# Kernel tuning notes

Hardware: AMD Instinct MI355X
Metric: run time of the kernel (lower is better)

## Reference

```python
import jax, jax.numpy as jnp
import numpy as np

B, C, H, W = 64, 512, 7, 7        # x4: dim_b=512, layer4 spatial 7x7
HY, WY = 28, 28                   # y (x1): layer1 56x56 -> cov1 stride2 -> 28x28
NUM_HEADS = 8
HEAD_DIM = C // NUM_HEADS
SCALE = HEAD_DIM ** -0.5
K1, K2 = 2, 3
LN_EPS = 1e-5


def _avgpool_same(y, k, p):
    # torch nn.AvgPool2d(kernel=k, stride=1, padding=p), count_include_pad=True
    s = jax.lax.reduce_window(y, 0.0, jax.lax.add, (1, 1, k, k), (1, 1, 1, 1),
                              [(0, 0), (0, 0), (p, p), (p, p)])
    return s / float(k * k)


def setup_inputs() -> dict:
    key = jax.random.key(0)
    ks = jax.random.split(key, 8)
    x = jax.random.normal(ks[0], (B, C, H, W), dtype=jnp.float32)
    y = jax.random.normal(ks[1], (B, C, HY, WY), dtype=jnp.float32)
    # Linear weights stored as [in, out] (apply via x @ W)
    Wq = jax.random.normal(ks[2], (C, C), dtype=jnp.float32) * 0.02
    Wkv = jax.random.normal(ks[3], (C, 2 * C), dtype=jnp.float32) * 0.02
    Wproj = jax.random.normal(ks[4], (C, C), dtype=jnp.float32) * 0.02
    bproj = jnp.zeros((C,), dtype=jnp.float32)
    gamma = jnp.ones((C,), dtype=jnp.float32)
    beta = jnp.zeros((C,), dtype=jnp.float32)
    attn_w1 = jnp.full((1,), 0.5, dtype=jnp.float32)
    attn_w2 = jnp.full((1,), 0.5, dtype=jnp.float32)
    return dict(x=x, y=y, Wq=Wq, Wkv=Wkv, Wproj=Wproj, bproj=bproj,
                gamma=gamma, beta=beta, attn_w1=attn_w1, attn_w2=attn_w2)


def _topk_masked_softmax(attn, kc):
    # torch: scatter top-kc indices into a 0/1 mask, then where(mask>0, attn, -inf).
    # Equivalent (tie-free, as with continuous random logits): keep entries >= kth value.
    thr = jax.lax.top_k(attn, kc)[0][..., -1:]
    masked = jnp.where(attn >= jax.lax.stop_gradient(thr), attn, -jnp.inf)
    return jax.nn.softmax(masked, axis=-1)


def reference(x, y, Wq, Wkv, Wproj, bproj, gamma, beta, attn_w1, attn_w2):
    # Multi-scale pooling on y (all stride 1, 'same' spatial size)
    y = _avgpool_same(y, 3, 1) + _avgpool_same(y, 5, 2) + _avgpool_same(y, 7, 3)
    N1 = HY * WY
    y = y.reshape(B, C, N1).transpose(0, 2, 1)          # [B, N1, C]
    # LayerNorm over C
    mu = jnp.mean(y, axis=-1, keepdims=True)
    var = jnp.var(y, axis=-1, keepdims=True)
    y = (y - mu) / jnp.sqrt(var + LN_EPS) * gamma + beta

    N = H * W
    xs = x.reshape(B, C, N).transpose(0, 2, 1)          # [B, N, C]

    kv = (y @ Wkv).reshape(B, N1, 2, NUM_HEADS, HEAD_DIM)
    kv = kv.transpose(2, 0, 3, 1, 4)                    # [2, B, h, N1, d]
    k, v = kv[0], kv[1]
    q = (xs @ Wq).reshape(B, N, NUM_HEADS, HEAD_DIM).transpose(0, 2, 1, 3)  # [B,h,N,d]

    attn = jnp.einsum('bhnd,bhmd->bhnm', q, k) * SCALE  # [B, h, N, N1]

    attn1 = _topk_masked_softmax(attn, N1 // K1)
    attn2 = _topk_masked_softmax(attn, N1 // K2)
    out1 = jnp.einsum('bhnm,bhmd->bhnd', attn1, v)
    out2 = jnp.einsum('bhnm,bhmd->bhnd', attn2, v)
    out = out1 * attn_w1 + out2 * attn_w2               # [B, h, N, d]

    out = out.transpose(0, 2, 1, 3).reshape(B, N, C)    # [B, N, C]
    out = out @ Wproj + bproj
    return out.transpose(0, 2, 1).reshape(B, C, H, W)
```

## Files before the change

### kernel.cpp

```cpp
#include <hip/hip_runtime.h>
#include <hip/hip_bf16.h>


typedef __hip_bfloat16 bf16;
using bf16x8 = __attribute__((ext_vector_type(8))) short;
using f32x4 = __attribute__((ext_vector_type(4))) float;

#define DI __device__ __forceinline__

DI unsigned short b2u(float f) {
  bf16 h = __float2bfloat16(f);
  return *reinterpret_cast<unsigned short*>(&h);
}
DI float u2f(short s) { return __uint_as_float(((unsigned int)(unsigned short)s) << 16); }

DI float unkey(unsigned int k) {
  unsigned int u = (k & 0x80000000u) ? (k & 0x7FFFFFFFu) : ~k;
  return __uint_as_float(u);
}

__global__ __launch_bounds__(256) void pool2t_kernel(const float* __restrict__ y,
                                                     bf16* __restrict__ pooledT) {
  const int b = blockIdx.x >> 6, cg = blockIdx.x & 63;
  const float* src = y + ((size_t)b * 512 + cg * 8) * 784;
  bf16* drow = pooledT + ((size_t)b * 784) * 512 + cg * 8;
  __shared__ float I[8][870];
  const int tid = threadIdx.x;
  for (int i = tid; i < 6272; i += 256) {
    int p = i / 784, j = i - p * 784;
    int r = j / 28, c = j - r * 28;
    I[p][(r + 1) * 30 + c + 1] = src[p * 784 + j];
  }
  for (int i = tid; i < 8 * 58; i += 256) {
    int p = i / 58, e = i - p * 58;
    if (e < 30) I[p][e] = 0.f;
    else I[p][(e - 29) * 30] = 0.f;
  }
  __syncthreads();
  if (tid < 224) {
    int p = tid / 28, r = tid - (tid / 28) * 28;
    float run = 0.f;
    float* row = &I[p][(r + 1) * 30 + 1];
#pragma unroll
    for (int c = 0; c < 28; ++c) { run += row[c]; row[c] = run; }
  }
  __syncthreads();
  if (tid < 224) {
    int p = tid / 28, c = tid - (tid / 28) * 28;
    float run = 0.f;
    float* col = &I[p][30 + c + 1];
#pragma unroll
    for (int r = 0; r < 28; ++r) { run += col[r * 30]; col[r * 30] = run; }
  }
  __syncthreads();
  for (int j = tid; j < 784; j += 256) {
    int r = j / 28, c = j - (j / 28) * 28;
    int r0[3], r1[3], c0[3], c1[3];
#pragma unroll
    for (int pk = 1; pk <= 3; ++pk) {
      r0[pk - 1] = max(r - pk, 0) * 30;
      r1[pk - 1] = (min(r + pk, 27) + 1) * 30;
      c0[pk - 1] = max(c - pk, 0);
      c1[pk - 1] = min(c + pk, 27) + 1;
    }
    unsigned int u[4];
#pragma unroll
    for (int q = 0; q < 4; ++q) {
      float vv[2];
#pragma unroll
      for (int t = 0; t < 2; ++t) {
        const float* Ip = I[q * 2 + t];
        float acc = 0.f;
#pragma unroll
        for (int k = 0; k < 3; ++k) {
          float s = Ip[r1[k] + c1[k]] - Ip[r0[k] + c1[k]] - Ip[r1[k] + c0[k]] + Ip[r0[k] + c0[k]];
          acc += s * ((k == 0) ? (1.f / 9.f) : (k == 1) ? (1.f / 25.f) : (1.f / 49.f));
        }
        vv[t] = acc;
      }
      u[q] = (unsigned int)b2u(vv[0]) | ((unsigned int)b2u(vv[1]) << 16);
    }
    *reinterpret_cast<uint4*>(drow + (size_t)j * 512) = make_uint4(u[0], u[1], u[2], u[3]);
  }
}

__global__ __launch_bounds__(256) void lnrow_kernel(const bf16* __restrict__ pooledT,
                                                    const float* __restrict__ gamma,
                                                    const float* __restrict__ beta,
                                                    bf16* __restrict__ yln) {
  const int row = blockIdx.x * 4 + (threadIdx.x >> 6);
  const int lane = threadIdx.x & 63;
  bf16x8 raw = *reinterpret_cast<const bf16x8*>(pooledT + (size_t)row * 512 + lane * 8);
  float v[8];
  float s = 0.f, s2 = 0.f;
#pragma unroll
  for (int j = 0; j < 8; ++j) {
    v[j] = u2f(raw[j]);
    s += v[j];
    s2 += v[j] * v[j];
  }
#pragma unroll
  for (int off = 32; off; off >>= 1) {
    s += __shfl_xor(s, off, 64);
    s2 += __shfl_xor(s2, off, 64);
  }
  float mu = s * (1.f / 512.f);
  float rs = rsqrtf(s2 * (1.f / 512.f) - mu * mu + 1e-5f);
  float4 g0 = *reinterpret_cast<const float4*>(gamma + lane * 8);
  float4 g1 = *reinterpret_cast<const float4*>(gamma + lane * 8 + 4);
  float4 e0 = *reinterpret_cast<const float4*>(beta + lane * 8);
  float4 e1 = *reinterpret_cast<const float4*>(beta + lane * 8 + 4);
  float gg[8] = {g0.x, g0.y, g0.z, g0.w, g1.x, g1.y, g1.z, g1.w};
  float bb[8] = {e0.x, e0.y, e0.z, e0.w, e1.x, e1.y, e1.z, e1.w};
  unsigned int u[4];
#pragma unroll
  for (int q = 0; q < 4; ++q) {
    float o0 = (v[2 * q] - mu) * rs * gg[2 * q] + bb[2 * q];
    float o1 = (v[2 * q + 1] - mu) * rs * gg[2 * q + 1] + bb[2 * q + 1];
    u[q] = (unsigned int)b2u(o0) | ((unsigned int)b2u(o1) << 16);
  }
  *reinterpret_cast<uint4*>(yln + (size_t)row * 512 + lane * 8) = make_uint4(u[0], u[1], u[2], u[3]);
}

__global__ __launch_bounds__(256) void prep_kernel(const float* __restrict__ Wkv,
                                                   const float* __restrict__ Wq,
                                                   const float* __restrict__ Wproj,
                                                   const float* __restrict__ x,
                                                   bf16* __restrict__ wkvT, bf16* __restrict__ wqT,
                                                   bf16* __restrict__ wpT, bf16* __restrict__ xsTb,
                                                   bf16* __restrict__ Vt) {
  __shared__ float t[32][33];
  const int blk = blockIdx.x;
  const int tid = threadIdx.x;
  if (blk < 1024) {
    const float* W;
    bf16* WT;
    int N, bx, by;
    if (blk < 512) { W = Wkv; WT = wkvT; N = 1024; bx = blk & 31; by = blk >> 5; }
    else if (blk < 768) { W = Wq; WT = wqT; N = 512; bx = (blk - 512) & 15; by = (blk - 512) >> 4; }
    else { W = Wproj; WT = wpT; N = 512; bx = (blk - 768) & 15; by = (blk - 768) >> 4; }
    const int n0 = bx * 32, k0 = by * 32;
    for (int i = tid; i < 1024; i += 256) {
      int kr = i >> 5, nc = i & 31;
      t[kr][nc] = W[(size_t)(k0 + kr) * N + n0 + nc];
    }
    __syncthreads();
    for (int i = tid; i < 1024; i += 256) {
      int nr = i >> 5, kc = i & 31;
      WT[(size_t)(n0 + nr) * 512 + k0 + kc] = __float2bfloat16(t[kc][nr]);
    }
  } else if (blk < 7296) {
    int idx = (blk - 1024) * 256 + tid;
    int c = idx & 511;
    int rem = idx >> 9;
    int r = rem % 49, b = rem / 49;
    xsTb[idx] = __float2bfloat16(x[((size_t)b * 512 + c) * 49 + r]);
  } else {
    int idx = (blk - 7296) * 256 + tid;
    int row = idx >> 4, c = idx & 15;
    Vt[(size_t)row * 800 + 784 + c] = __float2bfloat16(0.f);
  }
}

#define GLD_LDS16(g, l)                                                              \
  __builtin_amdgcn_global_load_lds((const __attribute__((address_space(1))) unsigned int*)(g), \
                                   (__attribute__((address_space(3))) unsigned int*)(l), 16, 0, 0)

__global__ __launch_bounds__(256) void kv_mfma(const bf16* __restrict__ A,
                                               const bf16* __restrict__ Bt,
                                               bf16* __restrict__ Kb, bf16* __restrict__ Vt) {
  extern __shared__ __align__(16) bf16 smem[];
  bf16* As = smem;
  bf16* Bs = smem + 128 * 32;
  const int tid = threadIdx.x;
  const int lane = tid & 63;
  const int w = tid >> 6, wr = w >> 1, wc = w & 1;

  const int lin = blockIdx.y * 8 + blockIdx.x;
  const int c8 = lin & 7, j = lin >> 3;
  const int ex = j & 7, ey = c8 * 49 + (j >> 3);
  const int m0 = ey * 128, n0 = ex * 128;

  f32x4 acc[4][4];
#pragma unroll
  for (int m = 0; m < 4; ++m)
#pragma unroll
    for (int n = 0; n < 4; ++n) acc[m][n] = f32x4{0.f, 0.f, 0.f, 0.f};

  const int s0 = tid, s1 = tid + 256;
  const bf16* Ag0 = A + (size_t)(m0 + (s0 >> 2)) * 512 + (s0 & 3) * 8;
  const bf16* Ag1 = A + (size_t)(m0 + (s1 >> 2)) * 512 + (s1 & 3) * 8;
  const bf16* Bg0 = Bt + (size_t)(n0 + (s0 >> 2)) * 512 + (s0 & 3) * 8;
  const bf16* Bg1 = Bt + (size_t)(n0 + (s1 >> 2)) * 512 + (s1 & 3) * 8;
  bf16* Al0 = As + s0 * 8;
  bf16* Al1 = As + s1 * 8;
  bf16* Bl0 = Bs + s0 * 8;
  bf16* Bl1 = Bs + s1 * 8;

  const int fr = lane & 15;
  const int ko = (lane >> 4) * 8;
  const int rh = lane >> 4;

  for (int k0 = 0; k0 < 512; k0 += 32) {
    GLD_LDS16(Ag0 + k0, Al0);
    GLD_LDS16(Ag1 + k0, Al1);
    GLD_LDS16(Bg0 + k0, Bl0);
    GLD_LDS16(Bg1 + k0, Bl1);
    __syncthreads();
    bf16x8 af[4], bfr[4];
#pragma unroll
    for (int m = 0; m < 4; ++m)
      af[m] = *reinterpret_cast<const bf16x8*>(As + (wr * 64 + m * 16 + fr) * 32 + ko);
#pragma unroll
    for (int n = 0; n < 4; ++n)
      bfr[n] = *reinterpret_cast<const bf16x8*>(Bs + (wc * 64 + n * 16 + fr) * 32 + ko);
#pragma unroll
    for (int m = 0; m < 4; ++m)
#pragma unroll
      for (int n = 0; n < 4; ++n)
        acc[m][n] = __builtin_amdgcn_mfma_f32_16x16x32_bf16(af[m], bfr[n], acc[m][n], 0, 0, 0);
    __syncthreads();
  }

  if (n0 < 512) {
#pragma unroll
    for (int m = 0; m < 4; ++m) {
#pragma unroll
      for (int n = 0; n < 4; ++n) {
        int col = n0 + wc * 64 + n * 16 + fr;
        const size_t cbase = ((size_t)(col >> 6)) * (784 * 64) + (col & 63);
#pragma unroll
        for (int r = 0; r < 4; ++r) {
          int row = m0 + wr * 64 + m * 16 + rh * 4 + r;
          int b = row / 784, n1 = row - (row / 784) * 784;
          Kb[((size_t)b * 8) * (784 * 64) + cbase + (size_t)n1 * 64] = __float2bfloat16(acc[m][n][r]);
        }
      }
    }
  } else {
    bf16* stage = smem;
#pragma unroll
    for (int p = 0; p < 2; ++p) {
      __syncthreads();
      if (wr == p) {
#pragma unroll
        for (int m = 0; m < 4; ++m) {
#pragma unroll
          for (int n = 0; n < 4; ++n) {
            int coll = wc * 64 + n * 16 + fr;
            int rowl = m * 16 + rh * 4;
            unsigned int u0 = (unsigned int)b2u(acc[m][n][0]) | ((unsigned int)b2u(acc[m][n][1]) << 16);
            unsigned int u1 = (unsigned int)b2u(acc[m][n][2]) | ((unsigned int)b2u(acc[m][n][3]) << 16);
            *reinterpret_cast<uint2*>(stage + coll * 72 + rowl) = make_uint2(u0, u1);
          }
        }
      }
      __syncthreads();
      const int rbase = m0 + p * 64;
      for (int i = tid; i < 1024; i += 256) {
        int cc = i >> 3, tc = i & 7;
        int colg = n0 + cc;
        int h = (colg >> 6) & 7, d = colg & 63;
        int rs = rbase + tc * 8;
        int b = rs / 784, n1 = rs - b * 784;
        bf16x8 val = *reinterpret_cast<const bf16x8*>(stage + cc * 72 + tc * 8);
        bf16* dst = Vt + (((size_t)b * 8 + h) * 64 + d) * 800 + n1;
        if (n1 <= 776) {
          *reinterpret_cast<bf16x8*>(dst) = val;
        } else {
#pragma unroll
          for (int jj = 0; jj < 8; ++jj) {
            int rr = rs + jj;
            int bb2 = rr / 784, nn1 = rr - bb2 * 784;
            bf16 hv;
            *reinterpret_cast<short*>(&hv) = val[jj];
            Vt[(((size_t)bb2 * 8 + h) * 64 + d) * 800 + nn1] = hv;
          }
        }
      }
    }
  }
}

__global__ __launch_bounds__(256) void q_mfma(const bf16* __restrict__ A,
                                              const bf16* __restrict__ Bt,
                                              bf16* __restrict__ Qb) {
  __shared__ __align__(16) bf16 As[128 * 32];
  __shared__ __align__(16) bf16 Bs[128 * 32];
  const int tid = threadIdx.x;
  const int lane = tid & 63;
  const int w = tid >> 6, wr = w >> 1, wc = w & 1;
  const int m0 = blockIdx.y * 128, n0 = blockIdx.x * 128;

  f32x4 acc[4][4];
#pragma unroll
  for (int m = 0; m < 4; ++m)
#pragma unroll
    for (int n = 0; n < 4; ++n) acc[m][n] = f32x4{0.f, 0.f, 0.f, 0.f};

  const int s0 = tid, s1 = tid + 256;
  const bf16* Ag0 = A + (size_t)(m0 + (s0 >> 2)) * 512 + (s0 & 3) * 8;
  const bf16* Ag1 = A + (size_t)(m0 + (s1 >> 2)) * 512 + (s1 & 3) * 8;
  const bf16* Bg0 = Bt + (size_t)(n0 + (s0 >> 2)) * 512 + (s0 & 3) * 8;
  const bf16* Bg1 = Bt + (size_t)(n0 + (s1 >> 2)) * 512 + (s1 & 3) * 8;
  bf16* Al0 = As + s0 * 8;
  bf16* Al1 = As + s1 * 8;
  bf16* Bl0 = Bs + s0 * 8;
  bf16* Bl1 = Bs + s1 * 8;

  const int fr = lane & 15;
  const int ko = (lane >> 4) * 8;
  const int rh = lane >> 4;

  for (int k0 = 0; k0 < 512; k0 += 32) {
    GLD_LDS16(Ag0 + k0, Al0);
    GLD_LDS16(Ag1 + k0, Al1);
    GLD_LDS16(Bg0 + k0, Bl0);
    GLD_LDS16(Bg1 + k0, Bl1);
    __syncthreads();
    bf16x8 af[4], bfr[4];
#pragma unroll
    for (int m = 0; m < 4; ++m)
      af[m] = *reinterpret_cast<const bf16x8*>(As + (wr * 64 + m * 16 + fr) * 32 + ko);
#pragma unroll
    for (int n = 0; n < 4; ++n)
      bfr[n] = *reinterpret_cast<const bf16x8*>(Bs + (wc * 64 + n * 16 + fr) * 32 + ko);
#pragma unroll
    for (int m = 0; m < 4; ++m)
#pragma unroll
      for (int n = 0; n < 4; ++n)
        acc[m][n] = __builtin_amdgcn_mfma_f32_16x16x32_bf16(af[m], bfr[n], acc[m][n], 0, 0, 0);
    __syncthreads();
  }

#pragma unroll
  for (int m = 0; m < 4; ++m) {
#pragma unroll
    for (int n = 0; n < 4; ++n) {
      int col = n0 + wc * 64 + n * 16 + fr;
      const size_t cbase = ((size_t)(col >> 6)) * (49 * 64) + (col & 63);
#pragma unroll
      for (int r = 0; r < 4; ++r) {
        int row = m0 + wr * 64 + m * 16 + rh * 4 + r;
        if (row < 3136) {
          int b = row / 49, rr = row - (row / 49) * 49;
          Qb[((size_t)b * 8) * (49 * 64) + cbase + (size_t)rr * 64] = __float2bfloat16(acc[m][n][r]);
        }
      }
    }
  }
}

__global__ __launch_bounds__(256) void proj_mfma(const bf16* __restrict__ A,
                                                 const bf16* __restrict__ Bt,
                                                 const float* __restrict__ bias,
                                                 float* __restrict__ out) {
  __shared__ __align__(16) bf16 As[128 * 32];
  __shared__ __align__(16) bf16 Bs[128 * 32];
  const int tid = threadIdx.x;
  const int lane = tid & 63;
  const int w = tid >> 6, wr = w >> 1, wc = w & 1;
  const int m0 = blockIdx.y * 128, n0 = blockIdx.x * 128;

  f32x4 acc[4][4];
#pragma unroll
  for (int m = 0; m < 4; ++m)
#pragma unroll
    for (int n = 0; n < 4; ++n) acc[m][n] = f32x4{0.f, 0.f, 0.f, 0.f};

  const int s0 = tid, s1 = tid + 256;
  const bf16* Ag0 = A + (size_t)(m0 + (s0 >> 2)) * 1024 + (s0 & 3) * 8;
  const bf16* Ag1 = A + (size_t)(m0 + (s1 >> 2)) * 1024 + (s1 & 3) * 8;
  const bf16* Bg0 = Bt + (size_t)(n0 + (s0 >> 2)) * 512 + (s0 & 3) * 8;
  const bf16* Bg1 = Bt + (size_t)(n0 + (s1 >> 2)) * 512 + (s1 & 3) * 8;
  bf16* Al0 = As + s0 * 8;
  bf16* Al1 = As + s1 * 8;
  bf16* Bl0 = Bs + s0 * 8;
  bf16* Bl1 = Bs + s1 * 8;

  const int fr = lane & 15;
  const int ko = (lane >> 4) * 8;
  const int rh = lane >> 4;

  for (int k0 = 0; k0 < 1024; k0 += 32) {
    GLD_LDS16(Ag0 + k0, Al0);
    GLD_LDS16(Ag1 + k0, Al1);
    GLD_LDS16(Bg0 + (k0 & 511), Bl0);
    GLD_LDS16(Bg1 + (k0 & 511), Bl1);
    __syncthreads();
    bf16x8 af[4], bfr[4];
#pragma unroll
    for (int m = 0; m < 4; ++m)
      af[m] = *reinterpret_cast<const bf16x8*>(As + (wr * 64 + m * 16 + fr) * 32 + ko);
#pragma unroll
    for (int n = 0; n < 4; ++n)
      bfr[n] = *reinterpret_cast<const bf16x8*>(Bs + (wc * 64 + n * 16 + fr) * 32 + ko);
#pragma unroll
    for (int m = 0; m < 4; ++m)
#pragma unroll
      for (int n = 0; n < 4; ++n)
        acc[m][n] = __builtin_amdgcn_mfma_f32_16x16x32_bf16(af[m], bfr[n], acc[m][n], 0, 0, 0);
    __syncthreads();
  }

#pragma unroll
  for (int m = 0; m < 4; ++m) {
#pragma unroll
    for (int n = 0; n < 4; ++n) {
      int col = n0 + wc * 64 + n * 16 + fr;
      float bv = bias[col];
#pragma unroll
      for (int r = 0; r < 4; ++r) {
        int row = m0 + wr * 64 + m * 16 + rh * 4 + r;
        if (row < 3136) {
          int b = row / 49, rr = row - (row / 49) * 49;
          out[((size_t)b * 512 + col) * 49 + rr] = acc[m][n][r] + bv;
        }
      }
    }
  }
}

__global__ __launch_bounds__(256, 7) void attn_kernel(const bf16* __restrict__ Qb,
                                                      const bf16* __restrict__ K,
                                                      const bf16* __restrict__ Vt,
                                                      const float* __restrict__ aw1p,
                                                      const float* __restrict__ aw2p,
                                                      bf16* __restrict__ aoutHL) {
  const int lin = blockIdx.x;
  const int wk = (lin & 7) * 448 + (lin >> 3);
  const int bh = wk / 7;
  const int chunk = wk - bh * 7;
  const int b = bh >> 3, h = bh & 7;
  const int r0 = chunk * 7;
  const int tid = threadIdx.x;
  const int lane = tid & 63, w = tid >> 6;
  __shared__ __align__(16) unsigned char sMem[21952];
  float* sLog = reinterpret_cast<float*>(sMem);
  bf16* sW = reinterpret_cast<bf16*>(sMem);

  const int fr = lane & 15, ko = (lane >> 4) * 8, rh = lane >> 4;

  const bf16* Qp = Qb + ((size_t)bh * 49 + r0) * 64;
  const int qrow = (fr < 7) ? fr : 6;
  const bf16x8 aq0 = *reinterpret_cast<const bf16x8*>(Qp + qrow * 64 + ko);
  const bf16x8 aq1 = *reinterpret_cast<const bf16x8*>(Qp + qrow * 64 + 32 + ko);

  const bf16* Kp = K + (size_t)bh * (784 * 64);
  {
    const int rbase = rh * 4;
    const bf16* kbase = Kp + (size_t)fr * 64 + ko;
    bf16x8 kq0[4], kq1[4];
#pragma unroll
    for (int s = 0; s < 4; ++s) {
      int nt = w + s * 4;
      int ntc = nt < 49 ? nt : 48;
      const bf16* kr = kbase + (size_t)ntc * 1024;
      kq0[s] = *reinterpret_cast<const bf16x8*>(kr);
      kq1[s] = *reinterpret_cast<const bf16x8*>(kr + 32);
    }
#pragma unroll
    for (int i = 0; i < 13; ++i) {
      const int s = i & 3;
      const int nt = w + i * 4;
      if (nt < 49) {
        f32x4 acc = {0.f, 0.f, 0.f, 0.f};
        acc = __builtin_amdgcn_mfma_f32_16x16x32_bf16(aq0, kq0[s], acc, 0, 0, 0);
        acc = __builtin_amdgcn_mfma_f32_16x16x32_bf16(aq1, kq1[s], acc, 0, 0, 0);
#pragma unroll
        for (int r = 0; r < 4; ++r) {
          int row = rbase + r;
          if (row < 7) sLog[row * 784 + nt * 16 + fr] = acc[r] * 0.125f;
        }
      }
      const int ntn = w + (i + 4) * 4;
      if (ntn < 49) {
        const bf16* kr = kbase + (size_t)ntn * 1024;
        kq0[s] = *reinterpret_cast<const bf16x8*>(kr);
        kq1[s] = *reinterpret_cast<const bf16x8*>(kr + 32);
      }
    }
  }
  __syncthreads();

  const int ra = w;
  const int rb = (w + 4 < 7) ? (w + 4) : w;
  float va[13], vb[13];
#pragma unroll
  for (int i = 0; i < 13; ++i) {
    int m = lane + i * 64;
    va[i] = (m < 784) ? sLog[ra * 784 + m] : -INFINITY;
    vb[i] = (m < 784) ? sLog[rb * 784 + m] : -INFINITY;
  }
  __syncthreads();

  float mxa = va[0], mxb = vb[0];
#pragma unroll
  for (int i = 1; i < 13; ++i) {
    mxa = fmaxf(mxa, va[i]);
    mxb = fmaxf(mxb, vb[i]);
  }
#pragma unroll
  for (int off = 32; off; off >>= 1) {
    mxa = fmaxf(mxa, __shfl_xor(mxa, off, 64));
    mxb = fmaxf(mxb, __shfl_xor(mxb, off, 64));
  }

  unsigned int t1a = 0u, t2a = 0u, t1b = 0u, t2b = 0u;
  bool d1a = false, d2a = false, d1b = false, d2b = false;
  for (int bit = 31; bit >= 0; --bit) {
    const unsigned int mb = 1u << bit;
    if (!d1a) {
      float cf = unkey(t1a | mb);
      int n = 0;
#pragma unroll
      for (int i = 0; i < 13; ++i) n += __popcll(__ballot(va[i] >= cf));
      if (n >= 392) { t1a |= mb; d1a = (n == 392); }
    }
    if (!d2a) {
      float cf = unkey(t2a | mb);
      int n = 0;
#pragma unroll
      for (int i = 0; i < 13; ++i) n += __popcll(__ballot(va[i] >= cf));
      if (n >= 261) { t2a |= mb; d2a = (n == 261); }
    }
    if (!d1b) {
      float cf = unkey(t1b | mb);
      int n = 0;
#pragma unroll
      for (int i = 0; i < 13; ++i) n += __popcll(__ballot(vb[i] >= cf));
      if (n >= 392) { t1b |= mb; d1b = (n == 392); }
    }
    if (!d2b) {
      float cf = unkey(t2b | mb);
      int n = 0;
#pragma unroll
      for (int i = 0; i < 13; ++i) n += __popcll(__ballot(vb[i] >= cf));
      if (n >= 261) { t2b |= mb; d2b = (n == 261); }
    }
    if (d1a & d2a & d1b & d2b) break;
  }
  const float T1a = unkey(t1a), T2a = unkey(t2a);
  const float T1b = unkey(t1b), T2b = unkey(t2b);

  const float aw1 = aw1p[0], aw2 = aw2p[0];
  float ea[13], eb[13];
  float z1a = 0.f, z2a = 0.f, z1b = 0.f, z2b = 0.f;
#pragma unroll
  for (int i = 0; i < 13; ++i) {
    ea[i] = __expf(va[i] - mxa);
    eb[i] = __expf(vb[i] - mxb);
    if (va[i] >= T1a) z1a += ea[i];
    if (va[i] >= T2a) z2a += ea[i];
    if (vb[i] >= T1b) z1b += eb[i];
    if (vb[i] >= T2b) z2b += eb[i];
  }
#pragma unroll
  for (int off = 32; off; off >>= 1) {
    z1a += __shfl_xor(z1a, off, 64);
    z2a += __shfl_xor(z2a, off, 64);
    z1b += __shfl_xor(z1b, off, 64);
    z2b += __shfl_xor(z2b, off, 64);
  }
  const float a1a = aw1 / z1a, a2a = aw2 / z2a;
  const float a1b = aw1 / z1b, a2b = aw2 / z2b;
#pragma unroll
  for (int i = 0; i < 13; ++i) {
    int m = lane + i * 64;
    if (m < 784) {
      float wa = ea[i] * (((va[i] >= T1a) ? a1a : 0.f) + ((va[i] >= T2a) ? a2a : 0.f));
      sW[ra * 808 + m] = __float2bfloat16(wa);
      float wb = eb[i] * (((vb[i] >= T1b) ? a1b : 0.f) + ((vb[i] >= T2b) ? a2b : 0.f));
      sW[rb * 808 + m] = __float2bfloat16(wb);
    }
  }
  if (lane < 16) {
    sW[ra * 808 + 784 + lane] = __float2bfloat16(0.f);
    sW[rb * 808 + 784 + lane] = __float2bfloat16(0.f);
  }

  const bf16* vbase = Vt + ((size_t)bh * 64 + w * 16 + fr) * 800;
  bf16x8 vq[4];
#pragma unroll
  for (int s = 0; s < 4; ++s)
    vq[s] = *reinterpret_cast<const bf16x8*>(vbase + s * 32 + ko);
  __syncthreads();

  const bf16* wrow = sW + ((fr < 7) ? fr : 7) * 808;
  f32x4 acc0 = {0.f, 0.f, 0.f, 0.f}, acc1 = {0.f, 0.f, 0.f, 0.f};
#pragma unroll
  for (int ks = 0; ks < 25; ++ks) {
    const int s = ks & 3;
    bf16x8 a = *reinterpret_cast<const bf16x8*>(wrow + ks * 32 + ko);
    if (ks & 1)
      acc1 = __builtin_amdgcn_mfma_f32_16x16x32_bf16(a, vq[s], acc1, 0, 0, 0);
    else
      acc0 = __builtin_amdgcn_mfma_f32_16x16x32_bf16(a, vq[s], acc0, 0, 0, 0);
    if (ks + 4 < 25)
      vq[s] = *reinterpret_cast<const bf16x8*>(vbase + (ks + 4) * 32 + ko);
  }
  acc0 += acc1;
#pragma unroll
  for (int r = 0; r < 4; ++r) {
    int row = rh * 4 + r;
    if (row < 7) {
      float v = acc0[r];
      bf16 hi = __float2bfloat16(v);
      bf16 lo = __float2bfloat16(v - __bfloat162float(hi));
      size_t base = ((size_t)(b * 49 + r0 + row)) * 1024 + h * 64 + w * 16 + fr;
      aoutHL[base] = hi;
      aoutHL[base + 512] = lo;
    }
  }
}

extern "C" void kernel_launch(void* const* d_in, const int* in_sizes, int n_in, void* d_out,
                              int out_size, void* d_ws, size_t ws_size, hipStream_t stream) {
  const float* x = (const float*)d_in[0];
  const float* y = (const float*)d_in[1];
  const float* Wq = (const float*)d_in[2];
  const float* Wkv = (const float*)d_in[3];
  const float* Wproj = (const float*)d_in[4];
  const float* bproj = (const float*)d_in[5];
  const float* gamma = (const float*)d_in[6];
  const float* beta = (const float*)d_in[7];
  const float* aw1 = (const float*)d_in[8];
  const float* aw2 = (const float*)d_in[9];
  float* out = (float*)d_out;

  char* w = (char*)d_ws;
  const size_t SZ = 51380224ull;
  const size_t SZV = 52428800ull;
  bf16* pooledT = (bf16*)(w);
  bf16* yln = (bf16*)(w + SZ);
  bf16* Kb = (bf16*)(w);
  bf16* Vt = (bf16*)(w + 2 * SZ);
  size_t off = 2 * SZ + SZV;
  bf16* xsTb = (bf16*)(w + off);    off += 3276800;
  bf16* Qb = (bf16*)(w + off);      off += 3276800;
  bf16* aoutHL = (bf16*)(w + off);  off += 6553600;
  bf16* wkvT = (bf16*)(w + off);    off += 1048576;
  bf16* wqT = (bf16*)(w + off);     off += 524288;
  bf16* wpT = (bf16*)(w + off);     off += 524288;

  prep_kernel<<<dim3(9344), dim3(256), 0, stream>>>(Wkv, Wq, Wproj, x, wkvT, wqT, wpT, xsTb, Vt);
  pool2t_kernel<<<dim3(4096), dim3(256), 0, stream>>>(y, pooledT);
  lnrow_kernel<<<dim3(12544), dim3(256), 0, stream>>>(pooledT, gamma, beta, yln);
  q_mfma<<<dim3(4, 25), dim3(256), 0, stream>>>(xsTb, wqT, Qb);
  kv_mfma<<<dim3(8, 392), dim3(256), 18432, stream>>>(yln, wkvT, Kb, Vt);
  attn_kernel<<<dim3(3584), dim3(256), 0, stream>>>(Qb, Kb, Vt, aw1, aw2, aoutHL);
  proj_mfma<<<dim3(4, 25), dim3(256), 0, stream>>>(aoutHL, wpT, bproj, out);
}
```

Measured before the change: 327.7 us.

## Merge prep with pooling and LayerNorm with Q GEMM into combined launches

Folds the weight/input prep and the multi-scale pooling into one launch, with the pooling blocks remapped across batches. LayerNorm rows and the Q projection GEMM are likewise merged into one launch, so independent work overlaps and two launches disappear. The attention logits buffer in shared memory also gets a row stride of 786 instead of 784, intended to reduce LDS bank conflicts. The merged kernels carry the union of their shared memory, which can lower occupancy for the lighter block types.

```diff
diff --git a/kernel.cpp b/kernel.cpp
--- a/kernel.cpp
+++ b/kernel.cpp
@@ -19,117 +19,17 @@
   return __uint_as_float(u);
 }
 
-__global__ __launch_bounds__(256) void pool2t_kernel(const float* __restrict__ y,
-                                                     bf16* __restrict__ pooledT) {
-  const int b = blockIdx.x >> 6, cg = blockIdx.x & 63;
-  const float* src = y + ((size_t)b * 512 + cg * 8) * 784;
-  bf16* drow = pooledT + ((size_t)b * 784) * 512 + cg * 8;
+#define GLD_LDS16(g, l)                                                              \
+  __builtin_amdgcn_global_load_lds((const __attribute__((address_space(1))) unsigned int*)(g), \
+                                   (__attribute__((address_space(3))) unsigned int*)(l), 16, 0, 0)
+
+__global__ __launch_bounds__(256) void prep_pool_kernel(
+    const float* __restrict__ Wkv, const float* __restrict__ Wq, const float* __restrict__ Wproj,
+    const float* __restrict__ x, const float* __restrict__ y, bf16* __restrict__ wkvT,
+    bf16* __restrict__ wqT, bf16* __restrict__ wpT, bf16* __restrict__ xsTb,
+    bf16* __restrict__ Vt, bf16* __restrict__ pooledT) {
+  __shared__ float t[32][33];
   __shared__ float I[8][870];
-  const int tid = threadIdx.x;
-  for (int i = tid; i < 6272; i += 256) {
-    int p = i / 784, j = i - p * 784;
-    int r = j / 28, c = j - r * 28;
-    I[p][(r + 1) * 30 + c + 1] = src[p * 784 + j];
-  }
-  for (int i = tid; i < 8 * 58; i += 256) {
-    int p = i / 58, e = i - p * 58;
-    if (e < 30) I[p][e] = 0.f;
-    else I[p][(e - 29) * 30] = 0.f;
-  }
-  __syncthreads();
-  if (tid < 224) {
-    int p = tid / 28, r = tid - (tid / 28) * 28;
-    float run = 0.f;
-    float* row = &I[p][(r + 1) * 30 + 1];
-#pragma unroll
-    for (int c = 0; c < 28; ++c) { run += row[c]; row[c] = run; }
-  }
-  __syncthreads();
-  if (tid < 224) {
-    int p = tid / 28, c = tid - (tid / 28) * 28;
-    float run = 0.f;
-    float* col = &I[p][30 + c + 1];
-#pragma unroll
-    for (int r = 0; r < 28; ++r) { run += col[r * 30]; col[r * 30] = run; }
-  }
-  __syncthreads();
-  for (int j = tid; j < 784; j += 256) {
-    int r = j / 28, c = j - (j / 28) * 28;
-    int r0[3], r1[3], c0[3], c1[3];
-#pragma unroll
-    for (int pk = 1; pk <= 3; ++pk) {
-      r0[pk - 1] = max(r - pk, 0) * 30;
-      r1[pk - 1] = (min(r + pk, 27) + 1) * 30;
-      c0[pk - 1] = max(c - pk, 0);
-      c1[pk - 1] = min(c + pk, 27) + 1;
-    }
-    unsigned int u[4];
-#pragma unroll
-    for (int q = 0; q < 4; ++q) {
-      float vv[2];
-#pragma unroll
-      for (int t = 0; t < 2; ++t) {
-        const float* Ip = I[q * 2 + t];
-        float acc = 0.f;
-#pragma unroll
-        for (int k = 0; k < 3; ++k) {
-          float s = Ip[r1[k] + c1[k]] - Ip[r0[k] + c1[k]] - Ip[r1[k] + c0[k]] + Ip[r0[k] + c0[k]];
-          acc += s * ((k == 0) ? (1.f / 9.f) : (k == 1) ? (1.f / 25.f) : (1.f / 49.f));
-        }
-        vv[t] = acc;
-      }
-      u[q] = (unsigned int)b2u(vv[0]) | ((unsigned int)b2u(vv[1]) << 16);
-    }
-    *reinterpret_cast<uint4*>(drow + (size_t)j * 512) = make_uint4(u[0], u[1], u[2], u[3]);
-  }
-}
-
-__global__ __launch_bounds__(256) void lnrow_kernel(const bf16* __restrict__ pooledT,
-                                                    const float* __restrict__ gamma,
-                                                    const float* __restrict__ beta,
-                                                    bf16* __restrict__ yln) {
-  const int row = blockIdx.x * 4 + (threadIdx.x >> 6);
-  const int lane = threadIdx.x & 63;
-  bf16x8 raw = *reinterpret_cast<const bf16x8*>(pooledT + (size_t)row * 512 + lane * 8);
-  float v[8];
-  float s = 0.f, s2 = 0.f;
-#pragma unroll
-  for (int j = 0; j < 8; ++j) {
-    v[j] = u2f(raw[j]);
-    s += v[j];
-    s2 += v[j] * v[j];
-  }
-#pragma unroll
-  for (int off = 32; off; off >>= 1) {
-    s += __shfl_xor(s, off, 64);
-    s2 += __shfl_xor(s2, off, 64);
-  }
-  float mu = s * (1.f / 512.f);
-  float rs = rsqrtf(s2 * (1.f / 512.f) - mu * mu + 1e-5f);
-  float4 g0 = *reinterpret_cast<const float4*>(gamma + lane * 8);
-  float4 g1 = *reinterpret_cast<const float4*>(gamma + lane * 8 + 4);
-  float4 e0 = *reinterpret_cast<const float4*>(beta + lane * 8);
-  float4 e1 = *reinterpret_cast<const float4*>(beta + lane * 8 + 4);
-  float gg[8] = {g0.x, g0.y, g0.z, g0.w, g1.x, g1.y, g1.z, g1.w};
-  float bb[8] = {e0.x, e0.y, e0.z, e0.w, e1.x, e1.y, e1.z, e1.w};
-  unsigned int u[4];
-#pragma unroll
-  for (int q = 0; q < 4; ++q) {
-    float o0 = (v[2 * q] - mu) * rs * gg[2 * q] + bb[2 * q];
-    float o1 = (v[2 * q + 1] - mu) * rs * gg[2 * q + 1] + bb[2 * q + 1];
-    u[q] = (unsigned int)b2u(o0) | ((unsigned int)b2u(o1) << 16);
-  }
-  *reinterpret_cast<uint4*>(yln + (size_t)row * 512 + lane * 8) = make_uint4(u[0], u[1], u[2], u[3]);
-}
-
-__global__ __launch_bounds__(256) void prep_kernel(const float* __restrict__ Wkv,
-                                                   const float* __restrict__ Wq,
-                                                   const float* __restrict__ Wproj,
-                                                   const float* __restrict__ x,
-                                                   bf16* __restrict__ wkvT, bf16* __restrict__ wqT,
-                                                   bf16* __restrict__ wpT, bf16* __restrict__ xsTb,
-                                                   bf16* __restrict__ Vt) {
-  __shared__ float t[32][33];
   const int blk = blockIdx.x;
   const int tid = threadIdx.x;
   if (blk < 1024) {
@@ -155,16 +55,179 @@
     int rem = idx >> 9;
     int r = rem % 49, b = rem / 49;
     xsTb[idx] = __float2bfloat16(x[((size_t)b * 512 + c) * 49 + r]);
-  } else {
+  } else if (blk < 9344) {
     int idx = (blk - 7296) * 256 + tid;
     int row = idx >> 4, c = idx & 15;
     Vt[(size_t)row * 800 + 784 + c] = __float2bfloat16(0.f);
-  }
-}
-
-#define GLD_LDS16(g, l)                                                              \
-  __builtin_amdgcn_global_load_lds((const __attribute__((address_space(1))) unsigned int*)(g), \
-                                   (__attribute__((address_space(3))) unsigned int*)(l), 16, 0, 0)
+  } else {
+    const int p = blk - 9344;
+    const int wk = (p & 7) * 512 + (p >> 3);
+    const int b = wk >> 6, cg = wk & 63;
+    const float* src = y + ((size_t)b * 512 + cg * 8) * 784;
+    bf16* drow = pooledT + ((size_t)b * 784) * 512 + cg * 8;
+    for (int i = tid; i < 6272; i += 256) {
+      int pp = i / 784, j = i - pp * 784;
+      int r = j / 28, c = j - r * 28;
+      I[pp][(r + 1) * 30 + c + 1] = src[pp * 784 + j];
+    }
+    for (int i = tid; i < 8 * 58; i += 256) {
+      int pp = i / 58, e = i - pp * 58;
+      if (e < 30) I[pp][e] = 0.f;
+      else I[pp][(e - 29) * 30] = 0.f;
+    }
+    __syncthreads();
+    if (tid < 224) {
+      int pp = tid / 28, r = tid - (tid / 28) * 28;
+      float run = 0.f;
+      float* row = &I[pp][(r + 1) * 30 + 1];
+#pragma unroll
+      for (int c = 0; c < 28; ++c) { run += row[c]; row[c] = run; }
+    }
+    __syncthreads();
+    if (tid < 224) {
+      int pp = tid / 28, c = tid - (tid / 28) * 28;
+      float run = 0.f;
+      float* col = &I[pp][30 + c + 1];
+#pragma unroll
+      for (int r = 0; r < 28; ++r) { run += col[r * 30]; col[r * 30] = run; }
+    }
+    __syncthreads();
+    for (int j = tid; j < 784; j += 256) {
+      int r = j / 28, c = j - (j / 28) * 28;
+      int r0[3], r1[3], c0[3], c1[3];
+#pragma unroll
+      for (int pk = 1; pk <= 3; ++pk) {
+        r0[pk - 1] = max(r - pk, 0) * 30;
+        r1[pk - 1] = (min(r + pk, 27) + 1) * 30;
+        c0[pk - 1] = max(c - pk, 0);
+        c1[pk - 1] = min(c + pk, 27) + 1;
+      }
+      unsigned int u[4];
+#pragma unroll
+      for (int q = 0; q < 4; ++q) {
+        float vv[2];
+#pragma unroll
+        for (int tt = 0; tt < 2; ++tt) {
+          const float* Ip = I[q * 2 + tt];
+          float acc = 0.f;
+#pragma unroll
+          for (int k = 0; k < 3; ++k) {
+            float s = Ip[r1[k] + c1[k]] - Ip[r0[k] + c1[k]] - Ip[r1[k] + c0[k]] + Ip[r0[k] + c0[k]];
+            acc += s * ((k == 0) ? (1.f / 9.f) : (k == 1) ? (1.f / 25.f) : (1.f / 49.f));
+          }
+          vv[tt] = acc;
+        }
+        u[q] = (unsigned int)b2u(vv[0]) | ((unsigned int)b2u(vv[1]) << 16);
+      }
+      *reinterpret_cast<uint4*>(drow + (size_t)j * 512) = make_uint4(u[0], u[1], u[2], u[3]);
+    }
+  }
+}
+
+__global__ __launch_bounds__(256) void ln_q_kernel(const bf16* __restrict__ pooledT,
+                                                   const float* __restrict__ gamma,
+                                                   const float* __restrict__ beta,
+                                                   bf16* __restrict__ yln,
+                                                   const bf16* __restrict__ A,
+                                                   const bf16* __restrict__ Bt,
+                                                   bf16* __restrict__ Qb) {
+  __shared__ __align__(16) bf16 As[128 * 32];
+  __shared__ __align__(16) bf16 Bs[128 * 32];
+  const int blk = blockIdx.x;
+  const int tid = threadIdx.x;
+  if (blk < 100) {
+    const int lane = tid & 63;
+    const int w = tid >> 6, wr = w >> 1, wc = w & 1;
+    const int m0 = (blk >> 2) * 128, n0 = (blk & 3) * 128;
+    f32x4 acc[4][4];
+#pragma unroll
+    for (int m = 0; m < 4; ++m)
+#pragma unroll
+      for (int n = 0; n < 4; ++n) acc[m][n] = f32x4{0.f, 0.f, 0.f, 0.f};
+    const int s0 = tid, s1 = tid + 256;
+    const bf16* Ag0 = A + (size_t)(m0 + (s0 >> 2)) * 512 + (s0 & 3) * 8;
+    const bf16* Ag1 = A + (size_t)(m0 + (s1 >> 2)) * 512 + (s1 & 3) * 8;
+    const bf16* Bg0 = Bt + (size_t)(n0 + (s0 >> 2)) * 512 + (s0 & 3) * 8;
+    const bf16* Bg1 = Bt + (size_t)(n0 + (s1 >> 2)) * 512 + (s1 & 3) * 8;
+    bf16* Al0 = As + s0 * 8;
+    bf16* Al1 = As + s1 * 8;
+    bf16* Bl0 = Bs + s0 * 8;
+    bf16* Bl1 = Bs + s1 * 8;
+    const int fr = lane & 15;
+    const int ko = (lane >> 4) * 8;
+    const int rh = lane >> 4;
+    for (int k0 = 0; k0 < 512; k0 += 32) {
+      GLD_LDS16(Ag0 + k0, Al0);
+      GLD_LDS16(Ag1 + k0, Al1);
+      GLD_LDS16(Bg0 + k0, Bl0);
+      GLD_LDS16(Bg1 + k0, Bl1);
+      __syncthreads();
+      bf16x8 af[4], bfr[4];
+#pragma unroll
+      for (int m = 0; m < 4; ++m)
+        af[m] = *reinterpret_cast<const bf16x8*>(As + (wr * 64 + m * 16 + fr) * 32 + ko);
+#pragma unroll
+      for (int n = 0; n < 4; ++n)
+        bfr[n] = *reinterpret_cast<const bf16x8*>(Bs + (wc * 64 + n * 16 + fr) * 32 + ko);
+#pragma unroll
+      for (int m = 0; m < 4; ++m)
+#pragma unroll
+        for (int n = 0; n < 4; ++n)
+          acc[m][n] = __builtin_amdgcn_mfma_f32_16x16x32_bf16(af[m], bfr[n], acc[m][n], 0, 0, 0);
+      __syncthreads();
+    }
+#pragma unroll
+    for (int m = 0; m < 4; ++m) {
+#pragma unroll
+      for (int n = 0; n < 4; ++n) {
+        int col = n0 + wc * 64 + n * 16 + fr;
+        const size_t cbase = ((size_t)(col >> 6)) * (49 * 64) + (col & 63);
+#pragma unroll
+        for (int r = 0; r < 4; ++r) {
+          int row = m0 + wr * 64 + m * 16 + rh * 4 + r;
+          if (row < 3136) {
+            int b = row / 49, rr = row - (row / 49) * 49;
+            Qb[((size_t)b * 8) * (49 * 64) + cbase + (size_t)rr * 64] = __float2bfloat16(acc[m][n][r]);
+          }
+        }
+      }
+    }
+  } else {
+    const int row = (blk - 100) * 4 + (tid >> 6);
+    const int lane = tid & 63;
+    bf16x8 raw = *reinterpret_cast<const bf16x8*>(pooledT + (size_t)row * 512 + lane * 8);
+    float v[8];
+    float s = 0.f, s2 = 0.f;
+#pragma unroll
+    for (int j = 0; j < 8; ++j) {
+      v[j] = u2f(raw[j]);
+      s += v[j];
+      s2 += v[j] * v[j];
+    }
+#pragma unroll
+    for (int off = 32; off; off >>= 1) {
+      s += __shfl_xor(s, off, 64);
+      s2 += __shfl_xor(s2, off, 64);
+    }
+    float mu = s * (1.f / 512.f);
+    float rs = rsqrtf(s2 * (1.f / 512.f) - mu * mu + 1e-5f);
+    float4 g0 = *reinterpret_cast<const float4*>(gamma + lane * 8);
+    float4 g1 = *reinterpret_cast<const float4*>(gamma + lane * 8 + 4);
+    float4 e0 = *reinterpret_cast<const float4*>(beta + lane * 8);
+    float4 e1 = *reinterpret_cast<const float4*>(beta + lane * 8 + 4);
+    float gg[8] = {g0.x, g0.y, g0.z, g0.w, g1.x, g1.y, g1.z, g1.w};
+    float bb[8] = {e0.x, e0.y, e0.z, e0.w, e1.x, e1.y, e1.z, e1.w};
+    unsigned int u[4];
+#pragma unroll
+    for (int q = 0; q < 4; ++q) {
+      float o0 = (v[2 * q] - mu) * rs * gg[2 * q] + bb[2 * q];
+      float o1 = (v[2 * q + 1] - mu) * rs * gg[2 * q + 1] + bb[2 * q + 1];
+      u[q] = (unsigned int)b2u(o0) | ((unsigned int)b2u(o1) << 16);
+    }
+    *reinterpret_cast<uint4*>(yln + (size_t)row * 512 + lane * 8) =
+        make_uint4(u[0], u[1], u[2], u[3]);
+  }
+}
 
 __global__ __launch_bounds__(256) void kv_mfma(const bf16* __restrict__ A,
                                                const bf16* __restrict__ Bt,
@@ -276,75 +339,6 @@
             *reinterpret_cast<short*>(&hv) = val[jj];
             Vt[(((size_t)bb2 * 8 + h) * 64 + d) * 800 + nn1] = hv;
           }
-        }
-      }
-    }
-  }
-}
-
-__global__ __launch_bounds__(256) void q_mfma(const bf16* __restrict__ A,
-                                              const bf16* __restrict__ Bt,
-                                              bf16* __restrict__ Qb) {
-  __shared__ __align__(16) bf16 As[128 * 32];
-  __shared__ __align__(16) bf16 Bs[128 * 32];
-  const int tid = threadIdx.x;
-  const int lane = tid & 63;
-  const int w = tid >> 6, wr = w >> 1, wc = w & 1;
-  const int m0 = blockIdx.y * 128, n0 = blockIdx.x * 128;
-
-  f32x4 acc[4][4];
-#pragma unroll
-  for (int m = 0; m < 4; ++m)
-#pragma unroll
-    for (int n = 0; n < 4; ++n) acc[m][n] = f32x4{0.f, 0.f, 0.f, 0.f};
-
-  const int s0 = tid, s1 = tid + 256;
-  const bf16* Ag0 = A + (size_t)(m0 + (s0 >> 2)) * 512 + (s0 & 3) * 8;
-  const bf16* Ag1 = A + (size_t)(m0 + (s1 >> 2)) * 512 + (s1 & 3) * 8;
-  const bf16* Bg0 = Bt + (size_t)(n0 + (s0 >> 2)) * 512 + (s0 & 3) * 8;
-  const bf16* Bg1 = Bt + (size_t)(n0 + (s1 >> 2)) * 512 + (s1 & 3) * 8;
-  bf16* Al0 = As + s0 * 8;
-  bf16* Al1 = As + s1 * 8;
-  bf16* Bl0 = Bs + s0 * 8;
-  bf16* Bl1 = Bs + s1 * 8;
-
-  const int fr = lane & 15;
-  const int ko = (lane >> 4) * 8;
-  const int rh = lane >> 4;
-
-  for (int k0 = 0; k0 < 512; k0 += 32) {
-    GLD_LDS16(Ag0 + k0, Al0);
-    GLD_LDS16(Ag1 + k0, Al1);
-    GLD_LDS16(Bg0 + k0, Bl0);
-    GLD_LDS16(Bg1 + k0, Bl1);
-    __syncthreads();
-    bf16x8 af[4], bfr[4];
-#pragma unroll
-    for (int m = 0; m < 4; ++m)
-      af[m] = *reinterpret_cast<const bf16x8*>(As + (wr * 64 + m * 16 + fr) * 32 + ko);
-#pragma unroll
-    for (int n = 0; n < 4; ++n)
-      bfr[n] = *reinterpret_cast<const bf16x8*>(Bs + (wc * 64 + n * 16 + fr) * 32 + ko);
-#pragma unroll
-    for (int m = 0; m < 4; ++m)
-#pragma unroll
-      for (int n = 0; n < 4; ++n)
-        acc[m][n] = __builtin_amdgcn_mfma_f32_16x16x32_bf16(af[m], bfr[n], acc[m][n], 0, 0, 0);
-    __syncthreads();
-  }
-
-#pragma unroll
-  for (int m = 0; m < 4; ++m) {
-#pragma unroll
-    for (int n = 0; n < 4; ++n) {
-      int col = n0 + wc * 64 + n * 16 + fr;
-      const size_t cbase = ((size_t)(col >> 6)) * (49 * 64) + (col & 63);
-#pragma unroll
-      for (int r = 0; r < 4; ++r) {
-        int row = m0 + wr * 64 + m * 16 + rh * 4 + r;
-        if (row < 3136) {
-          int b = row / 49, rr = row - (row / 49) * 49;
-          Qb[((size_t)b * 8) * (49 * 64) + cbase + (size_t)rr * 64] = __float2bfloat16(acc[m][n][r]);
         }
       }
     }
@@ -435,7 +429,7 @@
   const int r0 = chunk * 7;
   const int tid = threadIdx.x;
   const int lane = tid & 63, w = tid >> 6;
-  __shared__ __align__(16) unsigned char sMem[21952];
+  __shared__ __align__(16) unsigned char sMem[22008];
   float* sLog = reinterpret_cast<float*>(sMem);
   bf16* sW = reinterpret_cast<bf16*>(sMem);
 
@@ -470,7 +464,7 @@
 #pragma unroll
         for (int r = 0; r < 4; ++r) {
           int row = rbase + r;
-          if (row < 7) sLog[row * 784 + nt * 16 + fr] = acc[r] * 0.125f;
+          if (row < 7) sLog[row * 786 + nt * 16 + fr] = acc[r] * 0.125f;
         }
       }
       const int ntn = w + (i + 4) * 4;
@@ -489,8 +483,8 @@
 #pragma unroll
   for (int i = 0; i < 13; ++i) {
     int m = lane + i * 64;
-    va[i] = (m < 784) ? sLog[ra * 784 + m] : -INFINITY;
-    vb[i] = (m < 784) ? sLog[rb * 784 + m] : -INFINITY;
+    va[i] = (m < 784) ? sLog[ra * 786 + m] : -INFINITY;
+    vb[i] = (m < 784) ? sLog[rb * 786 + m] : -INFINITY;
   }
   __syncthreads();
 
@@ -643,10 +637,9 @@
   bf16* wqT = (bf16*)(w + off);     off += 524288;
   bf16* wpT = (bf16*)(w + off);     off += 524288;
 
-  prep_kernel<<<dim3(9344), dim3(256), 0, stream>>>(Wkv, Wq, Wproj, x, wkvT, wqT, wpT, xsTb, Vt);
-  pool2t_kernel<<<dim3(4096), dim3(256), 0, stream>>>(y, pooledT);
-  lnrow_kernel<<<dim3(12544), dim3(256), 0, stream>>>(pooledT, gamma, beta, yln);
-  q_mfma<<<dim3(4, 25), dim3(256), 0, stream>>>(xsTb, wqT, Qb);
+  prep_pool_kernel<<<dim3(13440), dim3(256), 0, stream>>>(Wkv, Wq, Wproj, x, y, wkvT, wqT, wpT,
+                                                          xsTb, Vt, pooledT);
+  ln_q_kernel<<<dim3(12644), dim3(256), 0, stream>>>(pooledT, gamma, beta, yln, xsTb, wqT, Qb);
   kv_mfma<<<dim3(8, 392), dim3(256), 18432, stream>>>(yln, wkvT, Kb, Vt);
   attn_kernel<<<dim3(3584), dim3(256), 0, stream>>>(Qb, Kb, Vt, aw1, aw2, aoutHL);
   proj_mfma<<<dim3(4, 25), dim3(256), 0, stream>>>(aoutHL, wpT, bproj, out);
```

Result: faster. 301.3 us (-8.0%).
